# Optimization experiments

Hardware: AMD Instinct MI355X
Metric: run time of the kernel (lower is better)

## Reference

```python
import jax, jax.numpy as jnp
import numpy as np

DIM, HEADS = 1024, 16
HEAD_DIM = DIM // HEADS
SCALE = HEAD_DIM ** -0.5


def setup_inputs() -> dict:
    key = jax.random.key(0)
    ks = jax.random.split(key, 5)
    B, N = 2, 2048
    x = jax.random.normal(ks[0], (B, N, DIM), dtype=jnp.float32)
    freqs = jax.random.normal(ks[1], (N, HEAD_DIM // 2), dtype=jnp.float32)
    w_qkv = jax.random.normal(ks[2], (3 * DIM, DIM), dtype=jnp.float32) * 0.02
    w_proj = jax.random.normal(ks[3], (DIM, DIM), dtype=jnp.float32) * 0.02
    b_proj = jnp.zeros((DIM,), dtype=jnp.float32)
    return {"x": x, "freqs": freqs, "w_qkv": w_qkv, "w_proj": w_proj, "b_proj": b_proj}


def _apply_rotary(t, cos, sin):
    # t: (B,N,H,D); cos/sin: (1,N,1,D//2)
    B, N, H, D = t.shape
    tp = t.reshape(B, N, H, D // 2, 2)
    x1, x2 = tp[..., 0], tp[..., 1]
    out = jnp.stack([x1 * cos - x2 * sin, x1 * sin + x2 * cos], axis=-1)
    return out.reshape(B, N, H, D)


def reference(x, freqs, w_qkv, w_proj, b_proj):
    B, N, C = x.shape
    H, D = HEADS, HEAD_DIM
    qkv = (x @ w_qkv.T).reshape(B, N, 3, H, D)  # fused QKV projection
    q, k, v = qkv[:, :, 0], qkv[:, :, 1], qkv[:, :, 2]  # each (B,N,H,D)
    cos = jnp.cos(freqs)[None, :, None, :]  # (1,N,1,D/2)
    sin = jnp.sin(freqs)[None, :, None, :]
    q = _apply_rotary(q, cos, sin)
    k = _apply_rotary(k, cos, sin)
    # SDPA: scores (B,H,N,N)
    scores = jnp.einsum("bqhd,bkhd->bhqk", q, k) * SCALE
    attn = jax.nn.softmax(scores, axis=-1)
    out = jnp.einsum("bhqk,bkhd->bqhd", attn, v).reshape(B, N, C)
    return out @ w_proj.T + b_proj
```

## Files before the change

kernel.cpp:

```cpp
#include <hip/hip_runtime.h>
#include <hip/hip_bf16.h>
#include <stdint.h>

#define BATCH   2
#define SEQ     2048
#define CDIM    1024
#define NHEAD   16
#define HDIM    64
#define MROWS   (BATCH*SEQ)
#define QKVN    (3*CDIM)
#define QSCALE  0.18033688011112042f

typedef __hip_bfloat16 bf16;
using bf16x8 = __attribute__((ext_vector_type(8))) __bf16;
using f32x4  = __attribute__((ext_vector_type(4))) float;
using s16x4  = __attribute__((ext_vector_type(4))) short;

__device__ __forceinline__ void gld16(const void* g, void* l) {
    __builtin_amdgcn_global_load_lds(
        (__attribute__((address_space(1))) void*)(void*)(g),
        (__attribute__((address_space(3))) void*)(l),
        16, 0, 0);
}

__device__ __forceinline__ f32x4 mfma16x16x32(bf16x8 a, bf16x8 b, f32x4 c) {
    return __builtin_amdgcn_mfma_f32_16x16x32_bf16(a, b, c, 0, 0, 0);
}
__device__ __forceinline__ f32x4 mfma16x16x16(s16x4 a, s16x4 b, f32x4 c) {
    return __builtin_amdgcn_mfma_f32_16x16x16bf16_1k(a, b, c, 0, 0, 0);
}

__device__ __forceinline__ uint16_t bfbits(float v) {
    bf16 b = __float2bfloat16(v);
    return *(uint16_t*)&b;
}
__device__ __forceinline__ uint32_t pkbf(float a, float b) {
    uint32_t au = __builtin_bit_cast(uint32_t, a);
    uint32_t bu = __builtin_bit_cast(uint32_t, b);
    return ((au + 0x8000u) >> 16) | ((bu + 0x8000u) & 0xffff0000u);
}
__device__ __forceinline__ void store_out(bf16* p, float v) { *p = __float2bfloat16(v); }
__device__ __forceinline__ void store_out(float* p, float v) { *p = v; }

#define NX_F4 ((size_t)MROWS*CDIM/4)
#define NQ_F4 ((size_t)QKVN*CDIM/4)
#define NP_F4 ((size_t)CDIM*CDIM/4)
#define NF_SC ((size_t)SEQ*32)

__global__ __launch_bounds__(256)
void cvt_kernel(const float* __restrict__ x, const float* __restrict__ wq,
                const float* __restrict__ wp, const float* __restrict__ freqs,
                bf16* __restrict__ xb, bf16* __restrict__ wqb,
                bf16* __restrict__ wpb, float2* __restrict__ csn) {
    size_t i4 = (size_t)blockIdx.x*256 + threadIdx.x;
    if (i4 < NX_F4 + NQ_F4 + NP_F4) {
        const float* src; bf16* dst; size_t off;
        if (i4 < NX_F4)           { src = x;  dst = xb;  off = i4; }
        else if (i4 < NX_F4+NQ_F4){ src = wq; dst = wqb; off = i4 - NX_F4; }
        else                      { src = wp; dst = wpb; off = i4 - NX_F4 - NQ_F4; }
        float4 v = ((const float4*)src)[off];
        bf16 o[4] = { __float2bfloat16(v.x), __float2bfloat16(v.y),
                      __float2bfloat16(v.z), __float2bfloat16(v.w) };
        *(uint64_t*)(dst + off*4) = *(const uint64_t*)o;
    } else if (i4 < NX_F4 + NQ_F4 + NP_F4 + NF_SC) {
        size_t k = i4 - (NX_F4 + NQ_F4 + NP_F4);
        float f = freqs[k];
        csn[k] = make_float2(cosf(f), sinf(f));
    }
}

__global__ __launch_bounds__(256)
void gemm_qkv_rope(const bf16* __restrict__ A, const bf16* __restrict__ Bw,
                   const float2* __restrict__ csn, bf16* __restrict__ Qr,
                   bf16* __restrict__ Kr, bf16* __restrict__ VG) {
    const int K = CDIM;
    __shared__ __align__(16) bf16 sh[64*136];
    bf16* As = sh;
    bf16* Bs = sh + 4096;

    const int bm = blockIdx.x, bn = blockIdx.y;
    const int tid  = threadIdx.x;
    const int lane = tid & 63;
    const int w    = tid >> 6;
    const int wm   = (w & 1) * 64;
    const int wn   = (w >> 1) * 64;
    const int quad = lane >> 4;
    const int l16  = lane & 15;

    const int c0 = tid, c1 = tid + 256;
    const size_t a_off0 = (size_t)(bm*128 + (c0 >> 2)) * K + (c0 & 3) * 8;
    const size_t a_off1 = (size_t)(bm*128 + (c1 >> 2)) * K + (c1 & 3) * 8;
    const size_t b_off0 = (size_t)(bn*128 + (c0 >> 2)) * K + (c0 & 3) * 8;
    const size_t b_off1 = (size_t)(bn*128 + (c1 >> 2)) * K + (c1 & 3) * 8;

    f32x4 acc[4][4] = {};

    for (int k0 = 0; k0 < K; k0 += 32) {
        __syncthreads();
        gld16(A + a_off0 + k0, &As[c0*8]);
        gld16(A + a_off1 + k0, &As[c1*8]);
        gld16(Bw + b_off0 + k0, &Bs[c0*8]);
        gld16(Bw + b_off1 + k0, &Bs[c1*8]);
        __syncthreads();

        bf16x8 af[4], bfv[4];
#pragma unroll
        for (int i = 0; i < 4; i++)
            af[i] = *(const bf16x8*)&As[(wm + i*16 + l16)*32 + quad*8];
#pragma unroll
        for (int i = 0; i < 4; i++)
            bfv[i] = *(const bf16x8*)&Bs[(wn + i*16 + l16)*32 + quad*8];
#pragma unroll
        for (int mi = 0; mi < 4; mi++)
#pragma unroll
            for (int ni = 0; ni < 4; ni++)
                acc[mi][ni] = mfma16x16x32(af[mi], bfv[ni], acc[mi][ni]);
    }

    const int region = bn >> 3;
    if (region < 2) {
        bf16* dst = region ? Kr : Qr;
        const float qs = region ? 1.0f : QSCALE;
        const int odd = l16 & 1;
#pragma unroll
        for (int mi = 0; mi < 4; mi++) {
#pragma unroll
            for (int ni = 0; ni < 4; ni++) {
                const int cq = (bn & 7)*128 + wn + ni*16 + l16;
                const int h = cq >> 6, d = cq & 63, fi = d >> 1;
#pragma unroll
                for (int r = 0; r < 4; r++) {
                    const int m = bm*128 + wm + mi*16 + quad*4 + r;
                    const int bb = m >> 11, n = m & 2047;
                    float own = acc[mi][ni][r];
                    float prt = __shfl_xor(own, 1);
                    float2 cs2 = csn[n*32 + fi];
                    float o = odd ? (prt*cs2.y + own*cs2.x)
                                  : (own*cs2.x - prt*cs2.y);
                    dst[((size_t)(bb*16 + h)*SEQ + n)*HDIM + d] =
                        __float2bfloat16(o * qs);
                }
            }
        }
    } else {
        const int bb = (bm*128) >> 11, n0l = (bm*128) & 2047;
        __syncthreads();
#pragma unroll
        for (int cc = 0; cc < 2; ++cc) {
            if ((w >> 1) == cc) {
#pragma unroll
                for (int mi = 0; mi < 4; mi++)
#pragma unroll
                    for (int ni = 0; ni < 4; ni++) {
                        const int d  = ni*16 + l16;
                        const int tl = wm + mi*16 + quad*4;
                        uint2 pk;
                        pk.x = (uint32_t)bfbits(acc[mi][ni][0]) |
                               ((uint32_t)bfbits(acc[mi][ni][1]) << 16);
                        pk.y = (uint32_t)bfbits(acc[mi][ni][2]) |
                               ((uint32_t)bfbits(acc[mi][ni][3]) << 16);
                        *(uint2*)&sh[d*136 + tl] = pk;
                    }
            }
            __syncthreads();
            const int h = (bn - 16)*2 + cc;
            bf16* vg = VG + (size_t)(bb*16 + h) * (SEQ*HDIM);
#pragma unroll
            for (int k = 0; k < 8; k++) {
                int s8   = tid + 256*k;
                int tile = s8 >> 10, si = s8 & 1023;
                int g  = si >> 6,  ln = si & 63;
                int j  = g >> 2,   dt = g & 3;
                int qk = ln >> 4,  ld = ln & 15;
                int tl = tile*64 + j*16 + qk*4;
                int d  = dt*16 + ld;
                *(uint2*)&vg[(size_t)((n0l >> 6) + tile)*4096 + si*4] =
                    *(const uint2*)&sh[d*136 + tl];
            }
            __syncthreads();
        }
    }
}

template<typename OutT, bool ADD_BIAS>
__global__ __launch_bounds__(256)
void gemm_bt(const bf16* __restrict__ A, const bf16* __restrict__ Bw,
             const float* __restrict__ bias, OutT* __restrict__ C,
             int M, int N, int K) {
    __shared__ __align__(16) bf16 As[128*32];
    __shared__ __align__(16) bf16 Bs[128*32];

    const int bm = blockIdx.x, bn = blockIdx.y;
    const int tid  = threadIdx.x;
    const int lane = tid & 63;
    const int w    = tid >> 6;
    const int wm   = (w & 1) * 64;
    const int wn   = (w >> 1) * 64;
    const int quad = lane >> 4;
    const int l16  = lane & 15;

    const int c0 = tid, c1 = tid + 256;
    const size_t a_off0 = (size_t)(bm*128 + (c0 >> 2)) * K + (c0 & 3) * 8;
    const size_t a_off1 = (size_t)(bm*128 + (c1 >> 2)) * K + (c1 & 3) * 8;
    const size_t b_off0 = (size_t)(bn*128 + (c0 >> 2)) * K + (c0 & 3) * 8;
    const size_t b_off1 = (size_t)(bn*128 + (c1 >> 2)) * K + (c1 & 3) * 8;

    f32x4 acc[4][4] = {};

    for (int k0 = 0; k0 < K; k0 += 32) {
        __syncthreads();
        gld16(A + a_off0 + k0, &As[c0*8]);
        gld16(A + a_off1 + k0, &As[c1*8]);
        gld16(Bw + b_off0 + k0, &Bs[c0*8]);
        gld16(Bw + b_off1 + k0, &Bs[c1*8]);
        __syncthreads();

        bf16x8 af[4], bfv[4];
#pragma unroll
        for (int i = 0; i < 4; i++)
            af[i] = *(const bf16x8*)&As[(wm + i*16 + l16)*32 + quad*8];
#pragma unroll
        for (int i = 0; i < 4; i++)
            bfv[i] = *(const bf16x8*)&Bs[(wn + i*16 + l16)*32 + quad*8];
#pragma unroll
        for (int mi = 0; mi < 4; mi++)
#pragma unroll
            for (int ni = 0; ni < 4; ni++)
                acc[mi][ni] = mfma16x16x32(af[mi], bfv[ni], acc[mi][ni]);
    }

#pragma unroll
    for (int mi = 0; mi < 4; mi++) {
        const int r0 = bm*128 + wm + mi*16 + quad*4;
#pragma unroll
        for (int ni = 0; ni < 4; ni++) {
            const int c = bn*128 + wn + ni*16 + l16;
            float bv = 0.f;
            if (ADD_BIAS) bv = bias[c];
#pragma unroll
            for (int r = 0; r < 4; r++)
                store_out(&C[(size_t)(r0 + r)*N + c], acc[mi][ni][r] + bv);
        }
    }
}

__global__ __launch_bounds__(64)
void attn_kernel(const bf16* __restrict__ Qr, const bf16* __restrict__ Kr,
                 const bf16* __restrict__ VG, bf16* __restrict__ Ao) {
    const int blk = blockIdx.x;
    const int bh  = blk >> 5;
    const int b   = bh >> 4, h = bh & 15;
    const int q0  = (blk & 31) * 64;
    const int lane = threadIdx.x;
    const int quad = lane >> 4, l16 = lane & 15;
    const int swz  = l16 & 7;

    __shared__ __align__(16) bf16 Ks[2][64*64];
    __shared__ __align__(16) bf16 Vs[2][64*64];

    bf16x8 qf[4][2];
#pragma unroll
    for (int t = 0; t < 4; t++) {
        const int qrow = q0 + t*16 + l16;
        const bf16* qp = Qr + ((size_t)bh*SEQ + qrow)*HDIM + quad*8;
        qf[t][0] = *(const bf16x8*)(qp);
        qf[t][1] = *(const bf16x8*)(qp + 32);
    }

    const bf16* KrB = Kr + (size_t)bh*SEQ*HDIM;
    const bf16* VgB = VG + (size_t)bh*SEQ*HDIM;
    int koff[8];
#pragma unroll
    for (int k = 0; k < 8; k++) {
        int c = lane + 64*k;
        int r = c >> 3, g = (c & 7) ^ (r & 7);
        koff[k] = r*HDIM + g*8;
    }

    f32x4 acc[4][4] = {};
    float lsum[4] = {};

#pragma unroll
    for (int k = 0; k < 8; k++) {
        gld16(KrB + koff[k], &Ks[0][(lane + 64*k)*8]);
        gld16(VgB + (lane + 64*k)*8, &Vs[0][(lane + 64*k)*8]);
    }

    for (int it = 0; it < SEQ/64; ++it) {
        const int cur = it & 1, nxt = cur ^ 1;
        bf16x8 kfr[4][2];
#pragma unroll
        for (int j = 0; j < 4; j++) {
            const bf16* krow = &Ks[cur][(j*16 + l16)*64];
            kfr[j][0] = *(const bf16x8*)(krow + ((quad     ^ swz) * 8));
            kfr[j][1] = *(const bf16x8*)(krow + (((quad+4) ^ swz) * 8));
        }
        s16x4 vfr[16];
#pragma unroll
        for (int m = 0; m < 16; m++)
            vfr[m] = *(const s16x4*)&Vs[cur][(m*64 + lane)*4];

        if (it + 1 < SEQ/64) {
            const size_t o = (size_t)(it + 1) * 4096;
#pragma unroll
            for (int k = 0; k < 8; k++) {
                gld16(KrB + koff[k] + o, &Ks[nxt][(lane + 64*k)*8]);
                gld16(VgB + (lane + 64*k)*8 + o, &Vs[nxt][(lane + 64*k)*8]);
            }
        }

        s16x4 pf[4][4];
#pragma unroll
        for (int j = 0; j < 4; j++) {
#pragma unroll
            for (int t = 0; t < 4; t++) {
                f32x4 sv = {};
                sv = mfma16x16x32(kfr[j][0], qf[t][0], sv);
                sv = mfma16x16x32(kfr[j][1], qf[t][1], sv);
                float e0 = __builtin_amdgcn_exp2f(sv[0]);
                float e1 = __builtin_amdgcn_exp2f(sv[1]);
                float e2 = __builtin_amdgcn_exp2f(sv[2]);
                float e3 = __builtin_amdgcn_exp2f(sv[3]);
                lsum[t] += (e0 + e1) + (e2 + e3);
                union { uint32_t u[2]; s16x4 v; } pa;
                pa.u[0] = pkbf(e0, e1);
                pa.u[1] = pkbf(e2, e3);
                pf[t][j] = pa.v;
            }
        }

#pragma unroll
        for (int dt = 0; dt < 4; dt++) {
#pragma unroll
            for (int j = 0; j < 4; j++) {
                s16x4 vf = vfr[j*4 + dt];
#pragma unroll
                for (int t = 0; t < 4; t++)
                    acc[t][dt] = mfma16x16x16(pf[t][j], vf, acc[t][dt]);
            }
        }
    }

#pragma unroll
    for (int t = 0; t < 4; t++) {
        lsum[t] += __shfl_xor(lsum[t], 16, 64);
        lsum[t] += __shfl_xor(lsum[t], 32, 64);
    }
    float lt[4][4];
#pragma unroll
    for (int t = 0; t < 4; t++)
#pragma unroll
        for (int r = 0; r < 4; r++)
            lt[t][r] = __shfl(lsum[t], quad*20 + r, 64);

#pragma unroll
    for (int t = 0; t < 4; t++)
#pragma unroll
        for (int dt = 0; dt < 4; dt++)
#pragma unroll
            for (int r = 0; r < 4; r++) {
                int qr  = q0 + t*16 + quad*4 + r;
                int col = h*HDIM + dt*16 + l16;
                Ao[(size_t)(b*SEQ + qr)*CDIM + col] =
                    __float2bfloat16(acc[t][dt][r] / lt[t][r]);
            }
}

extern "C" void kernel_launch(void* const* d_in, const int* in_sizes, int n_in,
                              void* d_out, int out_size, void* d_ws, size_t ws_size,
                              hipStream_t stream) {
    const float* x      = (const float*)d_in[0];
    const float* freqs  = (const float*)d_in[1];
    const float* w_qkv  = (const float*)d_in[2];
    const float* w_proj = (const float*)d_in[3];
    const float* b_proj = (const float*)d_in[4];
    float* out = (float*)d_out;

    char* ws = (char*)d_ws;
    bf16*   xb    = (bf16*)ws;   ws += (size_t)MROWS * CDIM * sizeof(bf16);
    bf16*   wqkvb = (bf16*)ws;   ws += (size_t)QKVN * CDIM * sizeof(bf16);
    bf16*   wprojb= (bf16*)ws;   ws += (size_t)CDIM * CDIM * sizeof(bf16);
    float2* csn   = (float2*)ws; ws += (size_t)SEQ * 32 * sizeof(float2);
    bf16*   Qr    = (bf16*)ws;   ws += (size_t)BATCH*NHEAD*SEQ*HDIM*sizeof(bf16);
    bf16*   Kr    = (bf16*)ws;   ws += (size_t)BATCH*NHEAD*SEQ*HDIM*sizeof(bf16);
    bf16*   VG    = (bf16*)ws;   ws += (size_t)BATCH*NHEAD*SEQ*HDIM*sizeof(bf16);
    bf16*   Ao    = (bf16*)ws;

    {
        size_t nthr = NX_F4 + NQ_F4 + NP_F4 + NF_SC;
        cvt_kernel<<<dim3((nthr + 255) / 256), dim3(256), 0, stream>>>(
            x, w_qkv, w_proj, freqs, xb, wqkvb, wprojb, csn);
    }
    gemm_qkv_rope<<<dim3(MROWS/128, QKVN/128), dim3(256), 0, stream>>>(
        xb, wqkvb, csn, Qr, Kr, VG);
    attn_kernel<<<dim3(BATCH*NHEAD*(SEQ/64)), dim3(64), 0, stream>>>(
        Qr, Kr, VG, Ao);
    gemm_bt<float, true><<<dim3(MROWS/128, CDIM/128), dim3(256), 0, stream>>>(
        Ao, wprojb, b_proj, out, MROWS, CDIM, CDIM);
}
```

Baseline: 211.2 us.

## Split attention key loop across two waves with LDS reduction

The attention block grows from one wave to two, and each wave processes half of the key/value sequence into its own single LDS buffer. The partial output accumulators and row sums are then added through LDS by one wave before normalization. This roughly halves the serial loop per block and adds wave-level parallelism. In exchange, the per-wave double buffering is replaced by an explicit wait each iteration, and a final reduction step is added.

```diff
diff --git a/kernel.cpp b/kernel.cpp
--- a/kernel.cpp
+++ b/kernel.cpp
@@ -244,14 +244,16 @@
     }
 }
 
-__global__ __launch_bounds__(64)
+__global__ __launch_bounds__(128)
 void attn_kernel(const bf16* __restrict__ Qr, const bf16* __restrict__ Kr,
                  const bf16* __restrict__ VG, bf16* __restrict__ Ao) {
     const int blk = blockIdx.x;
     const int bh  = blk >> 5;
     const int b   = bh >> 4, h = bh & 15;
     const int q0  = (blk & 31) * 64;
-    const int lane = threadIdx.x;
+    const int tid = threadIdx.x;
+    const int wid = tid >> 6;
+    const int lane = tid & 63;
     const int quad = lane >> 4, l16 = lane & 15;
     const int swz  = l16 & 7;
 
@@ -267,8 +269,10 @@
         qf[t][1] = *(const bf16x8*)(qp + 32);
     }
 
-    const bf16* KrB = Kr + (size_t)bh*SEQ*HDIM;
-    const bf16* VgB = VG + (size_t)bh*SEQ*HDIM;
+    const bf16* KrB = Kr + (size_t)bh*SEQ*HDIM + (size_t)wid*16*4096;
+    const bf16* VgB = VG + (size_t)bh*SEQ*HDIM + (size_t)wid*16*4096;
+    bf16* myK = Ks[wid];
+    bf16* myV = Vs[wid];
     int koff[8];
 #pragma unroll
     for (int k = 0; k < 8; k++) {
@@ -282,30 +286,32 @@
 
 #pragma unroll
     for (int k = 0; k < 8; k++) {
-        gld16(KrB + koff[k], &Ks[0][(lane + 64*k)*8]);
-        gld16(VgB + (lane + 64*k)*8, &Vs[0][(lane + 64*k)*8]);
-    }
-
-    for (int it = 0; it < SEQ/64; ++it) {
-        const int cur = it & 1, nxt = cur ^ 1;
+        gld16(KrB + koff[k], &myK[(lane + 64*k)*8]);
+        gld16(VgB + (lane + 64*k)*8, &myV[(lane + 64*k)*8]);
+    }
+
+    for (int it = 0; it < 16; ++it) {
+        asm volatile("s_waitcnt vmcnt(0)" ::: "memory");
+
         bf16x8 kfr[4][2];
 #pragma unroll
         for (int j = 0; j < 4; j++) {
-            const bf16* krow = &Ks[cur][(j*16 + l16)*64];
+            const bf16* krow = &myK[(j*16 + l16)*64];
             kfr[j][0] = *(const bf16x8*)(krow + ((quad     ^ swz) * 8));
             kfr[j][1] = *(const bf16x8*)(krow + (((quad+4) ^ swz) * 8));
         }
         s16x4 vfr[16];
 #pragma unroll
         for (int m = 0; m < 16; m++)
-            vfr[m] = *(const s16x4*)&Vs[cur][(m*64 + lane)*4];
-
-        if (it + 1 < SEQ/64) {
+            vfr[m] = *(const s16x4*)&myV[(m*64 + lane)*4];
+        asm volatile("s_waitcnt lgkmcnt(0)" ::: "memory");
+
+        if (it + 1 < 16) {
             const size_t o = (size_t)(it + 1) * 4096;
 #pragma unroll
             for (int k = 0; k < 8; k++) {
-                gld16(KrB + koff[k] + o, &Ks[nxt][(lane + 64*k)*8]);
-                gld16(VgB + (lane + 64*k)*8 + o, &Vs[nxt][(lane + 64*k)*8]);
+                gld16(KrB + koff[k] + o, &myK[(lane + 64*k)*8]);
+                gld16(VgB + (lane + 64*k)*8 + o, &myV[(lane + 64*k)*8]);
             }
         }
 
@@ -341,6 +347,31 @@
         }
     }
 
+    float* cb = (float*)&Ks[0][0];
+    float* lb = (float*)&Vs[0][0];
+    __syncthreads();
+    if (wid == 1) {
+#pragma unroll
+        for (int t = 0; t < 4; t++) {
+#pragma unroll
+            for (int dt = 0; dt < 4; dt++)
+                *(f32x4*)&cb[((t*4 + dt)*64 + lane)*4] = acc[t][dt];
+            lb[t*64 + lane] = lsum[t];
+        }
+    }
+    __syncthreads();
+    if (wid == 1) return;
+
+#pragma unroll
+    for (int t = 0; t < 4; t++) {
+#pragma unroll
+        for (int dt = 0; dt < 4; dt++) {
+            f32x4 o = *(const f32x4*)&cb[((t*4 + dt)*64 + lane)*4];
+            acc[t][dt] += o;
+        }
+        lsum[t] += lb[t*64 + lane];
+    }
+
 #pragma unroll
     for (int t = 0; t < 4; t++) {
         lsum[t] += __shfl_xor(lsum[t], 16, 64);
@@ -393,7 +424,7 @@
     }
     gemm_qkv_rope<<<dim3(MROWS/128, QKVN/128), dim3(256), 0, stream>>>(
         xb, wqkvb, csn, Qr, Kr, VG);
-    attn_kernel<<<dim3(BATCH*NHEAD*(SEQ/64)), dim3(64), 0, stream>>>(
+    attn_kernel<<<dim3(BATCH*NHEAD*(SEQ/64)), dim3(128), 0, stream>>>(
         Qr, Kr, VG, Ao);
     gemm_bt<float, true><<<dim3(MROWS/128, CDIM/128), dim3(256), 0, stream>>>(
         Ao, wprojb, b_proj, out, MROWS, CDIM, CDIM);
```

New measurement: 216.9 us. 1.03x slower.

## Load K/V directly into registers in attention; shrink projection GEMM M-tile

Applied to the files above, without the earlier changes.

The attention kernel stops staging K and V tiles through double-buffered LDS. It now reads K fragments straight from global memory into ping-pong register buffers prefetched one tile ahead, and reads V fragments directly from global each step. The score/PV loop is also reordered so each key sub-block's probabilities feed the PV MFMAs right away, which lowers live register pressure. Separately, the output projection GEMM uses 64-row M tiles, doubling the block count (256 to 512) for better CU occupancy, at the cost of less B-tile reuse and more global traffic.

```diff
diff --git a/kernel.cpp b/kernel.cpp
--- a/kernel.cpp
+++ b/kernel.cpp
@@ -39,8 +39,6 @@
     uint32_t bu = __builtin_bit_cast(uint32_t, b);
     return ((au + 0x8000u) >> 16) | ((bu + 0x8000u) & 0xffff0000u);
 }
-__device__ __forceinline__ void store_out(bf16* p, float v) { *p = __float2bfloat16(v); }
-__device__ __forceinline__ void store_out(float* p, float v) { *p = v; }
 
 #define NX_F4 ((size_t)MROWS*CDIM/4)
 #define NQ_F4 ((size_t)QKVN*CDIM/4)
@@ -182,64 +180,60 @@
     }
 }
 
-template<typename OutT, bool ADD_BIAS>
 __global__ __launch_bounds__(256)
-void gemm_bt(const bf16* __restrict__ A, const bf16* __restrict__ Bw,
-             const float* __restrict__ bias, OutT* __restrict__ C,
-             int M, int N, int K) {
-    __shared__ __align__(16) bf16 As[128*32];
+void gemm_proj(const bf16* __restrict__ A, const bf16* __restrict__ Bw,
+               const float* __restrict__ bias, float* __restrict__ C,
+               int M, int N, int K) {
+    __shared__ __align__(16) bf16 As[64*32];
     __shared__ __align__(16) bf16 Bs[128*32];
 
     const int bm = blockIdx.x, bn = blockIdx.y;
     const int tid  = threadIdx.x;
     const int lane = tid & 63;
     const int w    = tid >> 6;
-    const int wm   = (w & 1) * 64;
+    const int wm   = (w & 1) * 32;
     const int wn   = (w >> 1) * 64;
     const int quad = lane >> 4;
     const int l16  = lane & 15;
 
-    const int c0 = tid, c1 = tid + 256;
-    const size_t a_off0 = (size_t)(bm*128 + (c0 >> 2)) * K + (c0 & 3) * 8;
-    const size_t a_off1 = (size_t)(bm*128 + (c1 >> 2)) * K + (c1 & 3) * 8;
-    const size_t b_off0 = (size_t)(bn*128 + (c0 >> 2)) * K + (c0 & 3) * 8;
-    const size_t b_off1 = (size_t)(bn*128 + (c1 >> 2)) * K + (c1 & 3) * 8;
-
-    f32x4 acc[4][4] = {};
+    const int ca = tid, cb0 = tid, cb1 = tid + 256;
+    const size_t a_off  = (size_t)(bm*64  + (ca  >> 2)) * K + (ca  & 3) * 8;
+    const size_t b_off0 = (size_t)(bn*128 + (cb0 >> 2)) * K + (cb0 & 3) * 8;
+    const size_t b_off1 = (size_t)(bn*128 + (cb1 >> 2)) * K + (cb1 & 3) * 8;
+
+    f32x4 acc[2][4] = {};
 
     for (int k0 = 0; k0 < K; k0 += 32) {
         __syncthreads();
-        gld16(A + a_off0 + k0, &As[c0*8]);
-        gld16(A + a_off1 + k0, &As[c1*8]);
-        gld16(Bw + b_off0 + k0, &Bs[c0*8]);
-        gld16(Bw + b_off1 + k0, &Bs[c1*8]);
-        __syncthreads();
-
-        bf16x8 af[4], bfv[4];
-#pragma unroll
-        for (int i = 0; i < 4; i++)
+        gld16(A + a_off + k0, &As[ca*8]);
+        gld16(Bw + b_off0 + k0, &Bs[cb0*8]);
+        gld16(Bw + b_off1 + k0, &Bs[cb1*8]);
+        __syncthreads();
+
+        bf16x8 af[2], bfv[4];
+#pragma unroll
+        for (int i = 0; i < 2; i++)
             af[i] = *(const bf16x8*)&As[(wm + i*16 + l16)*32 + quad*8];
 #pragma unroll
         for (int i = 0; i < 4; i++)
             bfv[i] = *(const bf16x8*)&Bs[(wn + i*16 + l16)*32 + quad*8];
 #pragma unroll
-        for (int mi = 0; mi < 4; mi++)
+        for (int mi = 0; mi < 2; mi++)
 #pragma unroll
             for (int ni = 0; ni < 4; ni++)
                 acc[mi][ni] = mfma16x16x32(af[mi], bfv[ni], acc[mi][ni]);
     }
 
 #pragma unroll
-    for (int mi = 0; mi < 4; mi++) {
-        const int r0 = bm*128 + wm + mi*16 + quad*4;
+    for (int mi = 0; mi < 2; mi++) {
+        const int r0 = bm*64 + wm + mi*16 + quad*4;
 #pragma unroll
         for (int ni = 0; ni < 4; ni++) {
             const int c = bn*128 + wn + ni*16 + l16;
-            float bv = 0.f;
-            if (ADD_BIAS) bv = bias[c];
+            const float bv = bias[c];
 #pragma unroll
             for (int r = 0; r < 4; r++)
-                store_out(&C[(size_t)(r0 + r)*N + c], acc[mi][ni][r] + bv);
+                C[(size_t)(r0 + r)*N + c] = acc[mi][ni][r] + bv;
         }
     }
 }
@@ -253,10 +247,6 @@
     const int q0  = (blk & 31) * 64;
     const int lane = threadIdx.x;
     const int quad = lane >> 4, l16 = lane & 15;
-    const int swz  = l16 & 7;
-
-    __shared__ __align__(16) bf16 Ks[2][64*64];
-    __shared__ __align__(16) bf16 Vs[2][64*64];
 
     bf16x8 qf[4][2];
 #pragma unroll
@@ -269,54 +259,43 @@
 
     const bf16* KrB = Kr + (size_t)bh*SEQ*HDIM;
     const bf16* VgB = VG + (size_t)bh*SEQ*HDIM;
-    int koff[8];
-#pragma unroll
-    for (int k = 0; k < 8; k++) {
-        int c = lane + 64*k;
-        int r = c >> 3, g = (c & 7) ^ (r & 7);
-        koff[k] = r*HDIM + g*8;
-    }
 
     f32x4 acc[4][4] = {};
     float lsum[4] = {};
 
-#pragma unroll
-    for (int k = 0; k < 8; k++) {
-        gld16(KrB + koff[k], &Ks[0][(lane + 64*k)*8]);
-        gld16(VgB + (lane + 64*k)*8, &Vs[0][(lane + 64*k)*8]);
-    }
-
-    for (int it = 0; it < SEQ/64; ++it) {
-        const int cur = it & 1, nxt = cur ^ 1;
-        bf16x8 kfr[4][2];
+    bf16x8 kb0[4][2], kb1[4][2];
+
+#pragma unroll
+    for (int j = 0; j < 4; j++) {
+        const bf16* kr = KrB + (size_t)(j*16 + l16)*HDIM + quad*8;
+        kb0[j][0] = *(const bf16x8*)(kr);
+        kb0[j][1] = *(const bf16x8*)(kr + 32);
+    }
+
+    auto step = [&](bf16x8 (&kc)[4][2], bf16x8 (&kn)[4][2], int it) {
+        s16x4 vfr[16];
+        const bf16* vt = VgB + (size_t)it*4096;
+#pragma unroll
+        for (int m = 0; m < 16; m++)
+            vfr[m] = *(const s16x4*)&vt[(m*64 + lane)*4];
+
+        if (it + 1 < SEQ/64) {
+            const bf16* kr = KrB + (size_t)((it+1)*64 + l16)*HDIM + quad*8;
+#pragma unroll
+            for (int j = 0; j < 4; j++) {
+                kn[j][0] = *(const bf16x8*)(kr + j*16*HDIM);
+                kn[j][1] = *(const bf16x8*)(kr + j*16*HDIM + 32);
+            }
+        }
+
 #pragma unroll
         for (int j = 0; j < 4; j++) {
-            const bf16* krow = &Ks[cur][(j*16 + l16)*64];
-            kfr[j][0] = *(const bf16x8*)(krow + ((quad     ^ swz) * 8));
-            kfr[j][1] = *(const bf16x8*)(krow + (((quad+4) ^ swz) * 8));
-        }
-        s16x4 vfr[16];
-#pragma unroll
-        for (int m = 0; m < 16; m++)
-            vfr[m] = *(const s16x4*)&Vs[cur][(m*64 + lane)*4];
-
-        if (it + 1 < SEQ/64) {
-            const size_t o = (size_t)(it + 1) * 4096;
-#pragma unroll
-            for (int k = 0; k < 8; k++) {
-                gld16(KrB + koff[k] + o, &Ks[nxt][(lane + 64*k)*8]);
-                gld16(VgB + (lane + 64*k)*8 + o, &Vs[nxt][(lane + 64*k)*8]);
-            }
-        }
-
-        s16x4 pf[4][4];
-#pragma unroll
-        for (int j = 0; j < 4; j++) {
+            s16x4 pf[4];
 #pragma unroll
             for (int t = 0; t < 4; t++) {
                 f32x4 sv = {};
-                sv = mfma16x16x32(kfr[j][0], qf[t][0], sv);
-                sv = mfma16x16x32(kfr[j][1], qf[t][1], sv);
+                sv = mfma16x16x32(kc[j][0], qf[t][0], sv);
+                sv = mfma16x16x32(kc[j][1], qf[t][1], sv);
                 float e0 = __builtin_amdgcn_exp2f(sv[0]);
                 float e1 = __builtin_amdgcn_exp2f(sv[1]);
                 float e2 = __builtin_amdgcn_exp2f(sv[2]);
@@ -325,20 +304,21 @@
                 union { uint32_t u[2]; s16x4 v; } pa;
                 pa.u[0] = pkbf(e0, e1);
                 pa.u[1] = pkbf(e2, e3);
-                pf[t][j] = pa.v;
-            }
-        }
-
-#pragma unroll
-        for (int dt = 0; dt < 4; dt++) {
-#pragma unroll
-            for (int j = 0; j < 4; j++) {
+                pf[t] = pa.v;
+            }
+#pragma unroll
+            for (int dt = 0; dt < 4; dt++) {
                 s16x4 vf = vfr[j*4 + dt];
 #pragma unroll
                 for (int t = 0; t < 4; t++)
-                    acc[t][dt] = mfma16x16x16(pf[t][j], vf, acc[t][dt]);
-            }
-        }
+                    acc[t][dt] = mfma16x16x16(pf[t], vf, acc[t][dt]);
+            }
+        }
+    };
+
+    for (int it2 = 0; it2 < SEQ/128; ++it2) {
+        step(kb0, kb1, it2*2);
+        step(kb1, kb0, it2*2 + 1);
     }
 
 #pragma unroll
@@ -395,6 +375,6 @@
         xb, wqkvb, csn, Qr, Kr, VG);
     attn_kernel<<<dim3(BATCH*NHEAD*(SEQ/64)), dim3(64), 0, stream>>>(
         Qr, Kr, VG, Ao);
-    gemm_bt<float, true><<<dim3(MROWS/128, CDIM/128), dim3(256), 0, stream>>>(
+    gemm_proj<<<dim3(MROWS/64, CDIM/128), dim3(256), 0, stream>>>(
         Ao, wprojb, b_proj, out, MROWS, CDIM, CDIM);
 }
```

Result: slower. 229.2 us (+8.6%).
